# Optimization experiments

Measured on AMD Instinct MI355X. Metric: run time of the kernel, lower is better.

## Reference

```python
import jax, jax.numpy as jnp
import numpy as np

D_MODEL = 512
NHEAD = 8
HEAD_DIM = D_MODEL // NHEAD  # 64
ROTARY_DIM = HEAD_DIM        # rotary_dim defaults to head_dim
WINDOW = (127, 128)          # (left, right) sliding window, flash-attn convention
ROPE_BASE = 10000.0


def setup_inputs() -> dict:
    key = jax.random.key(0)
    k1, k2, k3, k4 = jax.random.split(key, 4)
    N, T = 4, 2048
    x = jax.random.normal(k1, (N, T, D_MODEL), dtype=jnp.float32)
    # Wqkv: Linear(d_model, 3*d_model, bias=False) -> weight [3*D, D]
    Wqkv_w = jax.random.normal(k2, (3 * D_MODEL, D_MODEL), dtype=jnp.float32) * (D_MODEL ** -0.5)
    # out_proj: Linear(d_model, d_model, bias=True)
    out_w = jax.random.normal(k3, (D_MODEL, D_MODEL), dtype=jnp.float32) * (D_MODEL ** -0.5)
    out_b = jax.random.normal(k4, (D_MODEL,), dtype=jnp.float32) * 0.01
    return {"x": x, "Wqkv_w": Wqkv_w, "out_w": out_w, "out_b": out_b}


def _rope_cos_sin(T, dtype):
    # flash-attn RotaryEmbedding: inv_freq over even indices of rotary_dim
    inv_freq = 1.0 / (ROPE_BASE ** (jnp.arange(0, ROTARY_DIM, 2, dtype=jnp.float32) / ROTARY_DIM))
    t = jnp.arange(T, dtype=jnp.float32)
    freqs = jnp.outer(t, inv_freq)  # [T, ROTARY_DIM//2]
    return jnp.cos(freqs).astype(dtype), jnp.sin(freqs).astype(dtype)


def _apply_rotary(x, cos, sin):
    # non-interleaved (rotate halves); x: [N, T, H, hd], rotary over first ROTARY_DIM dims
    r, rest = x[..., :ROTARY_DIM], x[..., ROTARY_DIM:]
    half = ROTARY_DIM // 2
    x1, x2 = r[..., :half], r[..., half:]
    c = cos[None, :, None, :]  # [1, T, 1, half]
    s = sin[None, :, None, :]
    rotated = jnp.concatenate([x1 * c - x2 * s, x2 * c + x1 * s], axis=-1)
    return jnp.concatenate([rotated, rest], axis=-1) if rest.shape[-1] else rotated


def reference(x, Wqkv_w, out_w, out_b):
    N, T, D = x.shape
    qkv = jnp.einsum('ntd,ed->nte', x, Wqkv_w).reshape(N, T, 3, NHEAD, HEAD_DIM)
    q, k, v = qkv[:, :, 0], qkv[:, :, 1], qkv[:, :, 2]  # each [N, T, H, hd]
    cos, sin = _rope_cos_sin(T, x.dtype)
    q = _apply_rotary(q, cos, sin)
    k = _apply_rotary(k, cos, sin)
    scale = HEAD_DIM ** -0.5
    scores = jnp.einsum('nthd,nshd->nhts', q, k) * scale  # [N, H, T, T]
    # sliding window: query i attends key j iff i - left <= j <= i + right
    i = jnp.arange(T)[:, None]
    j = jnp.arange(T)[None, :]
    mask = (j >= i - WINDOW[0]) & (j <= i + WINDOW[1])  # [T, T]
    scores = jnp.where(mask[None, None], scores, jnp.finfo(scores.dtype).min)
    attn = jax.nn.softmax(scores, axis=-1)
    ctx = jnp.einsum('nhts,nshd->nthd', attn, v).reshape(N, T, D)
    return jnp.einsum('ntd,ed->nte', ctx, out_w) + out_b
```

## Files before the change

### kernel.cpp

```cpp
#include <hip/hip_runtime.h>
#include <math.h>

#define TSEQ 2048
#define NB 4
#define DM 512
#define NH 8
#define HD 64

typedef _Float16 half8 __attribute__((ext_vector_type(8)));
typedef _Float16 half4 __attribute__((ext_vector_type(4)));
typedef float floatx4 __attribute__((ext_vector_type(4)));

#if __has_builtin(__builtin_amdgcn_exp2f)
#define EXP2F(x) __builtin_amdgcn_exp2f(x)
#else
#define EXP2F(x) exp2f(x)
#endif

__device__ __forceinline__ void gl2lds16(const _Float16* g, _Float16* l) {
  const __attribute__((address_space(1))) unsigned int* gp =
      (const __attribute__((address_space(1))) unsigned int*)(uintptr_t)g;
  __attribute__((address_space(3))) unsigned int* lp =
      (__attribute__((address_space(3))) unsigned int*)(uintptr_t)l;
  __builtin_amdgcn_global_load_lds(gp, lp, 16, 0, 0);
}


__device__ __forceinline__ void cvt8(const float* __restrict__ src, char* __restrict__ dst,
                                     int unit_src, int unit_dst) {
  const float4 a = ((const float4*)src)[2 * unit_src];
  const float4 b = ((const float4*)src)[2 * unit_src + 1];
  half8 h;
  h[0] = (_Float16)a.x; h[1] = (_Float16)a.y; h[2] = (_Float16)a.z; h[3] = (_Float16)a.w;
  h[4] = (_Float16)b.x; h[5] = (_Float16)b.y; h[6] = (_Float16)b.z; h[7] = (_Float16)b.w;
  *(half8*)(dst + (size_t)unit_dst * 16) = h;
}

__global__ void prep(const float* __restrict__ x, const float* __restrict__ wqkv,
                     const float* __restrict__ ow, char* __restrict__ ws) {
  const int i = blockIdx.x * 256 + threadIdx.x;
  if (i < 524288) {
    cvt8(x, ws, i, i);
  } else if (i < 622592) {
    const int o = i - 524288;
    cvt8(wqkv, ws + 8650752, o, o);
  } else if (i < 655360) {
    const int o = i - 622592;
    cvt8(ow, ws + 10485760, o, o);
  } else {
    const int u = i - 655360;
    float4 o4;
    {
      const int id = 2 * u, t = id >> 5, fi = id & 31;
      const float invf = powf(10000.0f, -(float)(2 * fi) * (1.0f / 64.0f));
      float s, c; sincosf((float)t * invf, &s, &c);
      o4.x = c; o4.y = s;
    }
    {
      const int id = 2 * u + 1, t = id >> 5, fi = id & 31;
      const float invf = powf(10000.0f, -(float)(2 * fi) * (1.0f / 64.0f));
      float s, c; sincosf((float)t * invf, &s, &c);
      o4.z = c; o4.w = s;
    }
    ((float4*)(ws + 46137344))[u] = o4;
  }
}

__global__ __launch_bounds__(512) void qkv_gemm_mfma(
    const _Float16* __restrict__ A, const _Float16* __restrict__ B,
    const float2* __restrict__ rope,
    _Float16* __restrict__ qb, _Float16* __restrict__ kb, _Float16* __restrict__ vT)
{
  __shared__ __align__(16) _Float16 As0[128 * 32];
  __shared__ __align__(16) _Float16 Bs0[128 * 32];
  __shared__ __align__(16) _Float16 As1[128 * 32];
  __shared__ __align__(16) _Float16 Bs1[128 * 32];
  const int tid = threadIdx.x;
  const int wv = tid >> 6, lane = tid & 63, quad = lane >> 4, col = lane & 15;
  const int wm = wv >> 1, we = wv & 1;
  const int m0 = blockIdx.x << 7, c0 = blockIdx.y << 7;
  const int r0 = tid >> 2, p0 = tid & 3;
  const int cA0 = (p0 - (r0 >> 1)) & 3;
  const _Float16* ga0 = &A[(size_t)(m0 + r0) * DM + cA0 * 8];
  const _Float16* gb0 = &B[(size_t)(c0 + r0) * DM + cA0 * 8];
  floatx4 acc[2][4] = {};

#define QKV_STAGE(AS, BS, K)                      \
  do {                                            \
    gl2lds16(ga0 + (K), &AS[tid * 8]);            \
    gl2lds16(gb0 + (K), &BS[tid * 8]);            \
  } while (0)

#define QKV_COMPUTE(AS, BS)                                                   \
  do {                                                                        \
    half8 af[2], bf[4];                                                       \
    _Pragma("unroll") for (int mt = 0; mt < 2; mt++) {                        \
      const int R = wm * 32 + mt * 16 + col;                                  \
      af[mt] = *(const half8*)&AS[R * 32 + (((quad + (R >> 1)) & 3) << 3)];   \
    }                                                                         \
    _Pragma("unroll") for (int et = 0; et < 4; et++) {                        \
      const int R = we * 64 + et * 16 + col;                                  \
      bf[et] = *(const half8*)&BS[R * 32 + (((quad + (R >> 1)) & 3) << 3)];   \
    }                                                                         \
    _Pragma("unroll") for (int mt = 0; mt < 2; mt++)                          \
      _Pragma("unroll") for (int et = 0; et < 4; et++)                        \
        acc[mt][et] =                                                         \
            __builtin_amdgcn_mfma_f32_16x16x32_f16(af[mt], bf[et], acc[mt][et], 0, 0, 0); \
  } while (0)

  QKV_STAGE(As0, Bs0, 0);
  for (int k0 = 0; k0 < DM; k0 += 64) {
    __syncthreads();
    QKV_STAGE(As1, Bs1, k0 + 32);
    QKV_COMPUTE(As0, Bs0);
    __syncthreads();
    if (k0 + 64 < DM) QKV_STAGE(As0, Bs0, k0 + 64);
    QKV_COMPUTE(As1, Bs1);
  }
#undef QKV_STAGE
#undef QKV_COMPUTE

  const int eidx = (c0 >> 6) + we;
  const int three = eidx >> 3, h = eidx & 7;
  const int mbase = m0 + wm * 32 + quad * 4;
  if (three == 2) {
#pragma unroll
    for (int mt = 0; mt < 2; mt++) {
      const int m = mbase + mt * 16;
      const int n = m >> 11, t = m & 2047;
#pragma unroll
      for (int et = 0; et < 4; et++) {
        const int dh = et * 16 + col;
        half4 hv;
#pragma unroll
        for (int r = 0; r < 4; r++) hv[r] = (_Float16)acc[mt][et][r];
        *(half4*)&vT[(size_t)(n * NH + h) * HD * TSEQ + (size_t)dh * TSEQ + t] = hv;
      }
    }
  } else {
    _Float16* dst = three ? kb : qb;
    const float scl = three ? 1.0f : 0.125f * 1.4426950408889634f;
#pragma unroll
    for (int mt = 0; mt < 2; mt++)
#pragma unroll
      for (int r = 0; r < 4; r++) {
        const int m = mbase + mt * 16 + r;
        const int n = m >> 11, t = m & 2047;
#pragma unroll
        for (int et = 0; et < 4; et++) {
          const int i = ((et & 1) << 4) + col;
          const float2 cs = rope[t * 32 + i];
          const float v = acc[mt][et][r];
          const float v2 = acc[mt][et ^ 2][r];
          const float o = (et < 2) ? (v * cs.x - v2 * cs.y) : (v * cs.x + v2 * cs.y);
          dst[((size_t)(n * NH + h) * TSEQ + t) * HD + et * 16 + col] = (_Float16)(o * scl);
        }
      }
  }
}

__global__ __launch_bounds__(512, 4) void attn_win_mfma(
    const _Float16* __restrict__ qb, const _Float16* __restrict__ kb,
    const _Float16* __restrict__ vT, _Float16* __restrict__ ctx)
{
  __shared__ __align__(16) char smem[55296];
  _Float16* Ks = (_Float16*)smem;
  _Float16* Vt = (_Float16*)(smem + 9216);
  _Float16* Ps = (_Float16*)(smem + 18432);
  _Float16* Osh = (_Float16*)(smem + 36864);

  const int tid = threadIdx.x;
  const int wv = tid >> 6;
  const int lane = tid & 63;
  const int quad = lane >> 4;
  const int col = lane & 15;
  const int lin = (blockIdx.y << 4) | blockIdx.x;
  const int sl  = ((lin & 7) << 6) | (lin >> 3);
  const int nh = sl >> 4;
  const int q0 = (sl & 15) << 7;
  const _Float16* qp = qb + (size_t)nh * TSEQ * HD;
  const _Float16* kp = kb + (size_t)nh * TSEQ * HD;
  const _Float16* vp = vT + (size_t)nh * HD * TSEQ;

  const int i_row = (wv << 4) + col;
  const int ig = q0 + i_row;
  const half8 qf0 = *(const half8*)&qp[(size_t)ig * HD + (quad << 3)];
  const half8 qf1 = *(const half8*)&qp[(size_t)ig * HD + 32 + (quad << 3)];

  float l_i = 0.0f;
  floatx4 accO[4] = {};

  const int kt0 = max(0, q0 - 127) >> 6;
  const int kt1 = min(TSEQ - 1, q0 + 255) >> 6;
  const int kr = tid >> 3, kc = (tid & 7) << 3;
  const _Float16* kpr = kp + (size_t)kr * HD + kc;
  const _Float16* vpr = vp + (size_t)kr * TSEQ + kc;
  const int iw0 = q0 + (wv << 4);

  half8 ck = *(const half8*)(kpr + (size_t)(kt0 << 6) * HD);
  half8 cv = *(const half8*)(vpr + (kt0 << 6));

  for (int kt = kt0; kt <= kt1; kt++) {
    const int j0 = kt << 6;
    __syncthreads();
    *(half8*)&Ks[kr * 72 + kc] = ck;
    *(half8*)&Vt[kr * 72 + kc] = cv;
    __syncthreads();

    {
      const int jn = (kt < kt1) ? (j0 + 64) : j0;
      ck = *(const half8*)(kpr + (size_t)jn * HD);
      cv = *(const half8*)(vpr + jn);
    }

    if ((unsigned)(j0 - iw0 + 190) >= 334u) continue;

    floatx4 S[4];
#pragma unroll
    for (int js = 0; js < 4; js++) {
      const int jlo = j0 + (js << 4);
      if ((unsigned)(jlo - iw0 + 142) < 286u) {
        const half8 a0 = *(const half8*)&Ks[((js << 4) + col) * 72 + (quad << 3)];
        const half8 a1 = *(const half8*)&Ks[((js << 4) + col) * 72 + 32 + (quad << 3)];
        floatx4 c = {0.f, 0.f, 0.f, 0.f};
        c = __builtin_amdgcn_mfma_f32_16x16x32_f16(a0, qf0, c, 0, 0, 0);
        c = __builtin_amdgcn_mfma_f32_16x16x32_f16(a1, qf1, c, 0, 0, 0);
        S[js] = c;
      }
    }
    const int relb = j0 - ig + 127 + (quad << 2);
#pragma unroll
    for (int js = 0; js < 4; js++) {
      const int jlo = j0 + (js << 4);
      if ((unsigned)(jlo - iw0 + 142) < 286u) {
        half4 ph;
#pragma unroll
        for (int r = 0; r < 4; r++) {
          const bool valid = (unsigned)(relb + (js << 4) + r) < 256u;
          const float p = valid ? EXP2F(S[js][r]) : 0.0f;
          l_i += p;
          ph[r] = (_Float16)p;
        }
        *(half4*)&Ps[i_row * 72 + (js << 4) + (quad << 2)] = ph;
      } else {
        const half4 zz = {(_Float16)0.f, (_Float16)0.f, (_Float16)0.f, (_Float16)0.f};
        *(half4*)&Ps[i_row * 72 + (js << 4) + (quad << 2)] = zz;
      }
    }
    const half8 pa0 = *(const half8*)&Ps[i_row * 72 + (quad << 3)];
    const half8 pa1 = *(const half8*)&Ps[i_row * 72 + 32 + (quad << 3)];
#pragma unroll
    for (int d4 = 0; d4 < 4; d4++) {
      const half8 vb0 = *(const half8*)&Vt[((d4 << 4) + col) * 72 + (quad << 3)];
      const half8 vb1 = *(const half8*)&Vt[((d4 << 4) + col) * 72 + 32 + (quad << 3)];
      accO[d4] = __builtin_amdgcn_mfma_f32_16x16x32_f16(pa0, vb0, accO[d4], 0, 0, 0);
      accO[d4] = __builtin_amdgcn_mfma_f32_16x16x32_f16(pa1, vb1, accO[d4], 0, 0, 0);
    }
  }
  l_i += __shfl_xor(l_i, 16, 64);
  l_i += __shfl_xor(l_i, 32, 64);
  {
    const float linv = 1.0f / l_i;
    float l4[4];
#pragma unroll
    for (int r = 0; r < 4; r++) l4[r] = __shfl(linv, (quad << 2) + r, 64);
#pragma unroll
    for (int d4 = 0; d4 < 4; d4++)
#pragma unroll
      for (int r = 0; r < 4; r++)
        Osh[((wv << 4) + (quad << 2) + r) * 72 + (d4 << 4) + col] = (_Float16)(accO[d4][r] * l4[r]);
  }
  __syncthreads();
  {
    const int n = nh >> 3, h = nh & 7;
    const int oi = tid >> 2, oc = (tid & 3) << 4;
    _Float16* dst = &ctx[((size_t)n * TSEQ + q0 + oi) * DM + h * HD + oc];
    *(half8*)&dst[0] = *(const half8*)&Osh[oi * 72 + oc];
    *(half8*)&dst[8] = *(const half8*)&Osh[oi * 72 + oc + 8];
  }
}

__global__ __launch_bounds__(512) void out_gemm_mfma(
    const _Float16* __restrict__ A, const _Float16* __restrict__ B,
    const float* __restrict__ bias, float* __restrict__ out)
{
  __shared__ __align__(16) _Float16 As0[128 * 32];
  __shared__ __align__(16) _Float16 Bs0[64 * 32];
  __shared__ __align__(16) _Float16 As1[128 * 32];
  __shared__ __align__(16) _Float16 Bs1[64 * 32];
  const int tid = threadIdx.x;
  const int wv = tid >> 6, lane = tid & 63, quad = lane >> 4, col = lane & 15;
  const int wm = wv >> 1, we = wv & 1;
  const int m0 = blockIdx.x << 7, c0 = blockIdx.y << 6;
  const int r0 = tid >> 2, p0 = tid & 3;
  const int cA0 = (p0 - (r0 >> 1)) & 3;
  const _Float16* ga0 = &A[(size_t)(m0 + r0) * DM + cA0 * 8];
  const _Float16* gb0 = &B[(size_t)(c0 + r0) * DM + cA0 * 8];
  floatx4 acc[2][2] = {};

#define OG_STAGE(AS, BS, K)                       \
  do {                                            \
    gl2lds16(ga0 + (K), &AS[tid * 8]);            \
    if (tid < 256) gl2lds16(gb0 + (K), &BS[tid * 8]); \
  } while (0)

#define OG_COMPUTE(AS, BS)                                                    \
  do {                                                                        \
    half8 af[2], bf[2];                                                       \
    _Pragma("unroll") for (int mt = 0; mt < 2; mt++) {                        \
      const int R = wm * 32 + mt * 16 + col;                                  \
      af[mt] = *(const half8*)&AS[R * 32 + (((quad + (R >> 1)) & 3) << 3)];   \
    }                                                                         \
    _Pragma("unroll") for (int et = 0; et < 2; et++) {                        \
      const int R = we * 32 + et * 16 + col;                                  \
      bf[et] = *(const half8*)&BS[R * 32 + (((quad + (R >> 1)) & 3) << 3)];   \
    }                                                                         \
    _Pragma("unroll") for (int mt = 0; mt < 2; mt++)                          \
      _Pragma("unroll") for (int et = 0; et < 2; et++)                        \
        acc[mt][et] =                                                         \
            __builtin_amdgcn_mfma_f32_16x16x32_f16(af[mt], bf[et], acc[mt][et], 0, 0, 0); \
  } while (0)

  OG_STAGE(As0, Bs0, 0);
  for (int k0 = 0; k0 < DM; k0 += 64) {
    __syncthreads();
    OG_STAGE(As1, Bs1, k0 + 32);
    OG_COMPUTE(As0, Bs0);
    __syncthreads();
    if (k0 + 64 < DM) OG_STAGE(As0, Bs0, k0 + 64);
    OG_COMPUTE(As1, Bs1);
  }
#undef OG_STAGE
#undef OG_COMPUTE

  float bb[2];
#pragma unroll
  for (int et = 0; et < 2; et++) bb[et] = bias[c0 + we * 32 + et * 16 + col];
  const int mbase = m0 + wm * 32 + quad * 4;
#pragma unroll
  for (int mt = 0; mt < 2; mt++)
#pragma unroll
    for (int r = 0; r < 4; r++) {
      const int m = mbase + mt * 16 + r;
#pragma unroll
      for (int et = 0; et < 2; et++)
        out[(size_t)m * DM + c0 + we * 32 + et * 16 + col] = acc[mt][et][r] + bb[et];
    }
}

extern "C" void kernel_launch(void* const* d_in, const int* in_sizes, int n_in,
                              void* d_out, int out_size, void* d_ws, size_t ws_size,
                              hipStream_t stream) {
  const float* x    = (const float*)d_in[0];
  const float* wqkv = (const float*)d_in[1];
  const float* ow   = (const float*)d_in[2];
  const float* ob   = (const float*)d_in[3];
  char* ws = (char*)d_ws;
  _Float16* xh    = (_Float16*)(ws);
  _Float16* wqkvh = (_Float16*)(ws + 8650752);
  _Float16* owh   = (_Float16*)(ws + 10485760);
  _Float16* qbuf  = (_Float16*)(ws + 11534336);
  _Float16* kbuf  = (_Float16*)(ws + 20971520);
  _Float16* vTb   = (_Float16*)(ws + 29360128);
  _Float16* ctxh  = (_Float16*)(ws + 37748736);
  float2*   rope  = (float2*)  (ws + 46137344);

  prep<<<2688, 256, 0, stream>>>(x, wqkv, ow, ws);
  qkv_gemm_mfma<<<dim3(64, 12), 512, 0, stream>>>(xh, wqkvh, rope, qbuf, kbuf, vTb);
  attn_win_mfma<<<dim3(16, 32), 512, 0, stream>>>(qbuf, kbuf, vTb, ctxh);
  out_gemm_mfma<<<dim3(64, 8), 512, 0, stream>>>(ctxh, owh, ob, (float*)d_out);
}
```

Baseline: 118.1 us.

## Double-buffer K/V tiles via direct global-to-LDS loads with XOR swizzle

The attention kernel now stages K and V^T tiles with global_load_lds into two ping-pong LDS buffers, prefetching the next tile while the current one is consumed. It replaces the old register-staged copy, which needed two barriers per iteration. Rows are no longer padded; an XOR chunk swizzle avoids bank conflicts instead. The output staging buffer now aliases the P buffer to shrink LDS. The main risk is load-completion ordering, since the code relies on __syncthreads to wait for the async LDS writes.

```diff
diff --git a/kernel.cpp b/kernel.cpp
--- a/kernel.cpp
+++ b/kernel.cpp
@@ -163,11 +163,13 @@
     const _Float16* __restrict__ qb, const _Float16* __restrict__ kb,
     const _Float16* __restrict__ vT, _Float16* __restrict__ ctx)
 {
-  __shared__ __align__(16) char smem[55296];
-  _Float16* Ks = (_Float16*)smem;
-  _Float16* Vt = (_Float16*)(smem + 9216);
-  _Float16* Ps = (_Float16*)(smem + 18432);
-  _Float16* Osh = (_Float16*)(smem + 36864);
+  __shared__ __align__(16) char smem[51200];
+  _Float16* const KsA = (_Float16*)smem;
+  _Float16* const VtA = (_Float16*)(smem + 8192);
+  _Float16* const KsB = (_Float16*)(smem + 16384);
+  _Float16* const VtB = (_Float16*)(smem + 24576);
+  _Float16* const Ps  = (_Float16*)(smem + 32768);
+  _Float16* const Osh = Ps;
 
   const int tid = threadIdx.x;
   const int wv = tid >> 6;
@@ -192,70 +194,77 @@
 
   const int kt0 = max(0, q0 - 127) >> 6;
   const int kt1 = min(TSEQ - 1, q0 + 255) >> 6;
-  const int kr = tid >> 3, kc = (tid & 7) << 3;
-  const _Float16* kpr = kp + (size_t)kr * HD + kc;
-  const _Float16* vpr = vp + (size_t)kr * TSEQ + kc;
+  const int srow = tid >> 3;
+  const int schunk = (tid & 7) ^ (srow & 7);
+  const _Float16* kpr = kp + (size_t)srow * HD + (schunk << 3);
+  const _Float16* vpr = vp + (size_t)srow * TSEQ + (schunk << 3);
   const int iw0 = q0 + (wv << 4);
 
-  half8 ck = *(const half8*)(kpr + (size_t)(kt0 << 6) * HD);
-  half8 cv = *(const half8*)(vpr + (kt0 << 6));
-
+  {
+    const int j0 = kt0 << 6;
+    gl2lds16(kpr + (size_t)j0 * HD, KsA + tid * 8);
+    gl2lds16(vpr + j0, VtA + tid * 8);
+  }
+  __syncthreads();
+
+  int p = 0;
   for (int kt = kt0; kt <= kt1; kt++) {
     const int j0 = kt << 6;
-    __syncthreads();
-    *(half8*)&Ks[kr * 72 + kc] = ck;
-    *(half8*)&Vt[kr * 72 + kc] = cv;
-    __syncthreads();
-
-    {
-      const int jn = (kt < kt1) ? (j0 + 64) : j0;
-      ck = *(const half8*)(kpr + (size_t)jn * HD);
-      cv = *(const half8*)(vpr + jn);
-    }
-
-    if ((unsigned)(j0 - iw0 + 190) >= 334u) continue;
-
-    floatx4 S[4];
-#pragma unroll
-    for (int js = 0; js < 4; js++) {
-      const int jlo = j0 + (js << 4);
-      if ((unsigned)(jlo - iw0 + 142) < 286u) {
-        const half8 a0 = *(const half8*)&Ks[((js << 4) + col) * 72 + (quad << 3)];
-        const half8 a1 = *(const half8*)&Ks[((js << 4) + col) * 72 + 32 + (quad << 3)];
-        floatx4 c = {0.f, 0.f, 0.f, 0.f};
-        c = __builtin_amdgcn_mfma_f32_16x16x32_f16(a0, qf0, c, 0, 0, 0);
-        c = __builtin_amdgcn_mfma_f32_16x16x32_f16(a1, qf1, c, 0, 0, 0);
-        S[js] = c;
-      }
-    }
-    const int relb = j0 - ig + 127 + (quad << 2);
-#pragma unroll
-    for (int js = 0; js < 4; js++) {
-      const int jlo = j0 + (js << 4);
-      if ((unsigned)(jlo - iw0 + 142) < 286u) {
-        half4 ph;
-#pragma unroll
-        for (int r = 0; r < 4; r++) {
-          const bool valid = (unsigned)(relb + (js << 4) + r) < 256u;
-          const float p = valid ? EXP2F(S[js][r]) : 0.0f;
-          l_i += p;
-          ph[r] = (_Float16)p;
+    const _Float16* Ksc = p ? KsB : KsA;
+    const _Float16* Vtc = p ? VtB : VtA;
+    if (kt < kt1) {
+      const int jn = j0 + 64;
+      gl2lds16(kpr + (size_t)jn * HD, (p ? KsA : KsB) + tid * 8);
+      gl2lds16(vpr + jn, (p ? VtA : VtB) + tid * 8);
+    }
+
+    if ((unsigned)(j0 - iw0 + 190) < 334u) {
+      floatx4 S[4];
+#pragma unroll
+      for (int js = 0; js < 4; js++) {
+        const int jlo = j0 + (js << 4);
+        if ((unsigned)(jlo - iw0 + 142) < 286u) {
+          const int R = (js << 4) + col;
+          const half8 a0 = *(const half8*)&Ksc[R * 64 + ((quad ^ (R & 7)) << 3)];
+          const half8 a1 = *(const half8*)&Ksc[R * 64 + (((quad + 4) ^ (R & 7)) << 3)];
+          floatx4 c = {0.f, 0.f, 0.f, 0.f};
+          c = __builtin_amdgcn_mfma_f32_16x16x32_f16(a0, qf0, c, 0, 0, 0);
+          c = __builtin_amdgcn_mfma_f32_16x16x32_f16(a1, qf1, c, 0, 0, 0);
+          S[js] = c;
         }
-        *(half4*)&Ps[i_row * 72 + (js << 4) + (quad << 2)] = ph;
-      } else {
-        const half4 zz = {(_Float16)0.f, (_Float16)0.f, (_Float16)0.f, (_Float16)0.f};
-        *(half4*)&Ps[i_row * 72 + (js << 4) + (quad << 2)] = zz;
-      }
-    }
-    const half8 pa0 = *(const half8*)&Ps[i_row * 72 + (quad << 3)];
-    const half8 pa1 = *(const half8*)&Ps[i_row * 72 + 32 + (quad << 3)];
-#pragma unroll
-    for (int d4 = 0; d4 < 4; d4++) {
-      const half8 vb0 = *(const half8*)&Vt[((d4 << 4) + col) * 72 + (quad << 3)];
-      const half8 vb1 = *(const half8*)&Vt[((d4 << 4) + col) * 72 + 32 + (quad << 3)];
-      accO[d4] = __builtin_amdgcn_mfma_f32_16x16x32_f16(pa0, vb0, accO[d4], 0, 0, 0);
-      accO[d4] = __builtin_amdgcn_mfma_f32_16x16x32_f16(pa1, vb1, accO[d4], 0, 0, 0);
-    }
+      }
+      const int relb = j0 - ig + 127 + (quad << 2);
+#pragma unroll
+      for (int js = 0; js < 4; js++) {
+        const int jlo = j0 + (js << 4);
+        if ((unsigned)(jlo - iw0 + 142) < 286u) {
+          half4 ph;
+#pragma unroll
+          for (int r = 0; r < 4; r++) {
+            const bool valid = (unsigned)(relb + (js << 4) + r) < 256u;
+            const float pv_ = valid ? EXP2F(S[js][r]) : 0.0f;
+            l_i += pv_;
+            ph[r] = (_Float16)pv_;
+          }
+          *(half4*)&Ps[i_row * 72 + (js << 4) + (quad << 2)] = ph;
+        } else {
+          const half4 zz = {(_Float16)0.f, (_Float16)0.f, (_Float16)0.f, (_Float16)0.f};
+          *(half4*)&Ps[i_row * 72 + (js << 4) + (quad << 2)] = zz;
+        }
+      }
+      const half8 pa0 = *(const half8*)&Ps[i_row * 72 + (quad << 3)];
+      const half8 pa1 = *(const half8*)&Ps[i_row * 72 + 32 + (quad << 3)];
+#pragma unroll
+      for (int d4 = 0; d4 < 4; d4++) {
+        const int D = (d4 << 4) + col;
+        const half8 vb0 = *(const half8*)&Vtc[D * 64 + ((quad ^ (D & 7)) << 3)];
+        const half8 vb1 = *(const half8*)&Vtc[D * 64 + (((quad + 4) ^ (D & 7)) << 3)];
+        accO[d4] = __builtin_amdgcn_mfma_f32_16x16x32_f16(pa0, vb0, accO[d4], 0, 0, 0);
+        accO[d4] = __builtin_amdgcn_mfma_f32_16x16x32_f16(pa1, vb1, accO[d4], 0, 0, 0);
+      }
+    }
+    __syncthreads();
+    p ^= 1;
   }
   l_i += __shfl_xor(l_i, 16, 64);
   l_i += __shfl_xor(l_i, 32, 64);
```

New measurement: 118.9 us (median of 2 runs). Within noise of the previous version (+0.6%).
